# Performance work log

Measured on AMD Instinct MI355X. Metric: run time of the kernel, lower is better.

## Reference

```python
import jax, jax.numpy as jnp
import numpy as np

D_MODEL = 2048
N_HEADS = 16
D_HEAD = D_MODEL // N_HEADS  # 128
D_KV = 512
D_ROPE = 64
D_SPLIT = D_HEAD - D_ROPE  # 64
ROPE_BASE = 10000.0
EPS = 1e-5


def _rmsnorm(x, g):
    var = jnp.mean(x * x, axis=-1, keepdims=True) + EPS
    return g * (x * jax.lax.rsqrt(var))


def _rope_cache(seq):
    # theta over d_head frequencies, sliced to d_rope//2 then tiled x2 (as in source)
    half_rope = D_ROPE // 2
    theta = 1.0 / (ROPE_BASE ** (jnp.arange(0, D_HEAD, 2, dtype=jnp.float32) / D_HEAD))
    idx_theta = jnp.arange(seq, dtype=jnp.float32)[:, None] * theta[None, :]  # [seq, d_head//2]
    cos = jnp.tile(jnp.cos(idx_theta[:, :half_rope]), (1, 2))  # [seq, d_rope]
    sin = jnp.tile(jnp.sin(idx_theta[:, :half_rope]), (1, 2))
    return cos[None, :, None, :], sin[None, :, None, :]  # [1,seq,1,d_rope]


def _apply_rope(x, cos, sin):
    # NOTE: source does rot_x = cat(x.chunk(2,-1), -1) which is the identity,
    # so faithfully: x*cos + x*sin
    return x * cos + x * sin


def setup_inputs() -> dict:
    key = jax.random.key(0)
    ks = jax.random.split(key, 12)
    def w(k, i, o):
        return jax.random.normal(k, (i, o), dtype=jnp.float32) * (1.0 / np.sqrt(i))
    return {
        "x": jax.random.normal(ks[0], (2, 2048, D_MODEL), dtype=jnp.float32),
        "W_dq": w(ks[1], D_MODEL, D_KV),
        "W_uq": w(ks[2], D_KV, N_HEADS * D_SPLIT),
        "W_dkv": w(ks[3], D_MODEL, D_KV),
        "W_uk": w(ks[4], D_KV, N_HEADS * D_SPLIT),
        "W_uv": w(ks[5], D_KV, N_HEADS * D_HEAD),
        "W_qr": w(ks[6], D_KV, N_HEADS * D_ROPE),
        "W_kr": w(ks[7], D_MODEL, N_HEADS * D_ROPE),
        "g_q": jnp.ones((D_KV,), dtype=jnp.float32),
        "g_kv": jnp.ones((D_KV,), dtype=jnp.float32),
        "W_out": w(ks[8], D_MODEL, D_MODEL),
        "b_out": jnp.zeros((D_MODEL,), dtype=jnp.float32),
    }


def reference(x, W_dq, W_uq, W_dkv, W_uk, W_uv, W_qr, W_kr, g_q, g_kv, W_out, b_out):
    batch, seq, _ = x.shape
    cos, sin = _rope_cache(seq)

    c_q = _rmsnorm(x @ W_dq, g_q)                                   # [b,s,d_kv]
    q_base = (c_q @ W_uq).reshape(batch, seq, N_HEADS, D_SPLIT)
    q_rot = _apply_rope((c_q @ W_qr).reshape(batch, seq, N_HEADS, D_ROPE), cos, sin)

    c_kv = _rmsnorm(x @ W_dkv, g_kv)
    k_base = (c_kv @ W_uk).reshape(batch, seq, N_HEADS, D_SPLIT)
    k_rot = _apply_rope((x @ W_kr).reshape(batch, seq, N_HEADS, D_ROPE), cos, sin)
    v = (c_kv @ W_uv).reshape(batch, seq, N_HEADS, D_HEAD)

    q = jnp.concatenate([q_base, q_rot], axis=-1)                   # [b,s,h,d_head]
    k = jnp.concatenate([k_base, k_rot], axis=-1)

    scale = jnp.sqrt(jnp.float32(D_HEAD))
    scores = jnp.einsum('bnhd,bmhd->bhnm', q, k) / scale            # [b,h,s,s]
    causal = jnp.tril(jnp.ones((seq, seq), dtype=bool))
    scores = jnp.where(causal[None, None], scores, -jnp.inf)
    attn = jax.nn.softmax(scores, axis=-1)
    out = jnp.einsum('bhnm,bmhd->bnhd', attn, v)                    # [b,s,h,d_head]
    out = out.reshape(batch, seq, D_MODEL)
    return out @ W_out + b_out
```

## Files before the change

### kernel.cpp

```cpp
#include <hip/hip_runtime.h>
#include <hip/hip_bf16.h>
#include <cstdint>

typedef __bf16 v8bf __attribute__((ext_vector_type(8)));
typedef float  v4f  __attribute__((ext_vector_type(4)));

__device__ __forceinline__ unsigned short b16(float f) {
  union { float f; unsigned u; } v; v.f = f;
  unsigned u = v.u;
  return (unsigned short)((u + 0x7fffu + ((u >> 16) & 1u)) >> 16);
}
__device__ __forceinline__ float bf2f(unsigned short u) {
  union { unsigned u; float f; } v; v.u = ((unsigned)u) << 16; return v.f;
}

#define GLOAD_LDS16(g, l)                                                     \
  __builtin_amdgcn_global_load_lds(                                           \
      (const __attribute__((address_space(1))) void*)(g),                     \
      (__attribute__((address_space(3))) void*)(l), 16, 0, 0)

__global__ __launch_bounds__(256) void conv_bf16(const float* __restrict__ in,
                                                 unsigned short* __restrict__ out) {
  size_t idx = (size_t)blockIdx.x * 256 + threadIdx.x;
  v4f v = *(const v4f*)(in + idx * 4);
  unsigned long long p = (unsigned long long)b16(v[0]) |
                         ((unsigned long long)b16(v[1]) << 16) |
                         ((unsigned long long)b16(v[2]) << 32) |
                         ((unsigned long long)b16(v[3]) << 48);
  *(unsigned long long*)(out + idx * 4) = p;
}

__global__ void transpose_w(const float* __restrict__ in, unsigned short* __restrict__ out,
                            int C, int R) {
  __shared__ float tile[32][33];
  int c0 = blockIdx.x * 32, r0 = blockIdx.y * 32;
  int x = threadIdx.x, y = threadIdx.y;
#pragma unroll
  for (int i = 0; i < 4; ++i)
    tile[y + 8 * i][x] = in[(size_t)(r0 + y + 8 * i) * C + c0 + x];
  __syncthreads();
#pragma unroll
  for (int i = 0; i < 4; ++i)
    out[(size_t)(c0 + y + 8 * i) * R + r0 + x] = b16(tile[x][y + 8 * i]);
}

__global__ void transpose_v(const unsigned short* __restrict__ T3, unsigned short* __restrict__ VT) {
  __shared__ unsigned short tile[32][34];
  int bh = blockIdx.z;
  int s0 = blockIdx.x * 32, d0 = blockIdx.y * 32;
  int x = threadIdx.x, y = threadIdx.y;
  const unsigned short* src = T3 + (size_t)(bh >> 4) * 2048 * 3072 + 1024 + (bh & 15) * 128;
#pragma unroll
  for (int i = 0; i < 4; ++i)
    tile[y + 8 * i][x] = src[(size_t)(s0 + y + 8 * i) * 3072 + d0 + x];
  __syncthreads();
  unsigned short* dst = VT + (size_t)bh * 128 * 2048;
#pragma unroll
  for (int i = 0; i < 4; ++i)
    dst[(size_t)(d0 + y + 8 * i) * 2048 + s0 + x] = tile[x][y + 8 * i];
}

template <int MODE>
__global__ __launch_bounds__(256) void gemm_bt(const unsigned short* __restrict__ A,
                                               const unsigned short* __restrict__ BT,
                                               void* __restrict__ C0,
                                               void* __restrict__ C1,
                                               const float* __restrict__ bias,
                                               int M, int N, int K) {
  __shared__ unsigned short As[128 * 32];
  __shared__ unsigned short Bs[128 * 32];
  const int tid = threadIdx.x;
  const int w = tid >> 6, l = tid & 63;
  const int wm = w >> 1, wn = w & 1;
  const int lg = l >> 4, lr = l & 15;
  const int nwg = gridDim.x * gridDim.y;
  const int f = blockIdx.y * gridDim.x + blockIdx.x;
  const int swz = (f & 7) * (nwg >> 3) + (f >> 3);
  const int m0 = (swz / gridDim.x) * 128, n0 = (swz % gridDim.x) * 128;

  const int srow = tid >> 2, scol = (tid & 3) * 8;
  const unsigned short* Ap0 = A  + (size_t)(m0 + srow) * K + scol;
  const unsigned short* Ap1 = A  + (size_t)(m0 + 64 + srow) * K + scol;
  const unsigned short* Bp0 = BT + (size_t)(n0 + srow) * K + scol;
  const unsigned short* Bp1 = BT + (size_t)(n0 + 64 + srow) * K + scol;
  unsigned short* Ad0 = As + tid * 8;
  unsigned short* Ad1 = As + 2048 + tid * 8;
  unsigned short* Bd0 = Bs + tid * 8;
  unsigned short* Bd1 = Bs + 2048 + tid * 8;

  v4f acc[4][4];
#pragma unroll
  for (int i = 0; i < 4; ++i)
#pragma unroll
    for (int j = 0; j < 4; ++j) acc[i][j] = (v4f){0.f, 0.f, 0.f, 0.f};

  for (int k0 = 0; k0 < K; k0 += 32) {
    GLOAD_LDS16(Ap0 + k0, Ad0);
    GLOAD_LDS16(Ap1 + k0, Ad1);
    GLOAD_LDS16(Bp0 + k0, Bd0);
    GLOAD_LDS16(Bp1 + k0, Bd1);
    __syncthreads();
    v8bf af[4], bfr[4];
#pragma unroll
    for (int mi = 0; mi < 4; ++mi)
      af[mi] = *(const v8bf*)&As[(wm * 64 + mi * 16 + lr) * 32 + lg * 8];
#pragma unroll
    for (int ni = 0; ni < 4; ++ni)
      bfr[ni] = *(const v8bf*)&Bs[(wn * 64 + ni * 16 + lr) * 32 + lg * 8];
#pragma unroll
    for (int mi = 0; mi < 4; ++mi)
#pragma unroll
      for (int ni = 0; ni < 4; ++ni)
        acc[mi][ni] = __builtin_amdgcn_mfma_f32_16x16x32_bf16(af[mi], bfr[ni], acc[mi][ni], 0, 0, 0);
    __syncthreads();
  }
#pragma unroll
  for (int mi = 0; mi < 4; ++mi)
#pragma unroll
    for (int ni = 0; ni < 4; ++ni) {
      const int col = n0 + wn * 64 + ni * 16 + lr;
#pragma unroll
      for (int rr = 0; rr < 4; ++rr) {
        const int row = m0 + wm * 64 + mi * 16 + lg * 4 + rr;
        const float v = acc[mi][ni][rr];
        if (MODE == 0) {
          ((float*)C0)[(size_t)row * N + col] = v + bias[col];
        } else if (MODE == 1) {
          ((unsigned short*)C0)[(size_t)row * N + col] = b16(v);
        } else if (MODE == 2) {
          if (col < 1024) {
            int qc = (col >> 6) * 128 + (col & 63);
            ((unsigned short*)C0)[(size_t)row * 2048 + qc] = b16(v);
          } else {
            int cc = col - 1024, d = cc & 63;
            int qc = (cc >> 6) * 128 + 64 + d;
            int s = row & 2047;
            float ang = (float)s * __expf(-(float)(d & 31) * 0.14391156831f);
            float sn, cs; __sincosf(ang, &sn, &cs);
            ((unsigned short*)C0)[(size_t)row * 2048 + qc] = b16(v * (cs + sn));
          }
        } else {
          if (col < 1024) {
            int kc = (col >> 6) * 128 + (col & 63);
            ((unsigned short*)C0)[(size_t)row * 2048 + kc] = b16(v);
          } else {
            ((unsigned short*)C1)[(size_t)row * 3072 + col] = b16(v);
          }
        }
      }
    }
}

__global__ __launch_bounds__(256) void rmsnorm_rope(const unsigned short* __restrict__ T1,
                                                    const float* __restrict__ gq,
                                                    const float* __restrict__ gkv,
                                                    unsigned short* __restrict__ cq,
                                                    unsigned short* __restrict__ ckv,
                                                    unsigned short* __restrict__ Kb) {
  const int row = blockIdx.x;
  const int t = threadIdx.x;
  const int s = row & 2047;
  const unsigned short* rp = T1 + (size_t)row * 2048;
  float xq0 = bf2f(rp[t]), xq1 = bf2f(rp[256 + t]);
  float xk0 = bf2f(rp[512 + t]), xk1 = bf2f(rp[768 + t]);
  float sq = xq0 * xq0 + xq1 * xq1;
  float sk = xk0 * xk0 + xk1 * xk1;
#pragma unroll
  for (int o = 1; o < 64; o <<= 1) { sq += __shfl_xor(sq, o); sk += __shfl_xor(sk, o); }
  __shared__ float red[8];
  if ((t & 63) == 0) { red[t >> 6] = sq; red[4 + (t >> 6)] = sk; }
  __syncthreads();
  float rq = rsqrtf((red[0] + red[1] + red[2] + red[3]) * (1.f / 512.f) + 1e-5f);
  float rk = rsqrtf((red[4] + red[5] + red[6] + red[7]) * (1.f / 512.f) + 1e-5f);
  cq[(size_t)row * 512 + t]        = b16(gq[t] * xq0 * rq);
  cq[(size_t)row * 512 + 256 + t]  = b16(gq[256 + t] * xq1 * rq);
  ckv[(size_t)row * 512 + t]       = b16(gkv[t] * xk0 * rk);
  ckv[(size_t)row * 512 + 256 + t] = b16(gkv[256 + t] * xk1 * rk);
#pragma unroll
  for (int i = 0; i < 4; ++i) {
    int j = t + 256 * i;
    int hh = j >> 6, d = j & 63;
    float ang = (float)s * __expf(-(float)(d & 31) * 0.14391156831f);
    float sn, cs; __sincosf(ang, &sn, &cs);
    Kb[(size_t)row * 2048 + hh * 128 + 64 + d] = b16(bf2f(rp[1024 + j]) * (cs + sn));
  }
}

__global__ __launch_bounds__(256) void flash_attn(const unsigned short* __restrict__ Qb,
                                                  const unsigned short* __restrict__ Kb,
                                                  const unsigned short* __restrict__ VTb,
                                                  unsigned short* __restrict__ Ob) {
  __shared__ unsigned short Ks[64 * 128];
  __shared__ unsigned short Vs[128 * 64];
  __shared__ unsigned short Ps[4 * 16 * 72];
  const int b = blockIdx.z, h = blockIdx.y;
  const int pj = blockIdx.x;
  const int tid = threadIdx.x;
  const int w = tid >> 6, l = tid & 63;
  const int lg = l >> 4, lr = l & 15;
  const float scale = 0.0883883476483184f;

  const unsigned short* Kbase = Kb + (size_t)b * 2048 * 2048 + h * 128;
  const unsigned short* Vbase = VTb + (size_t)(b * 16 + h) * 128 * 2048;

  for (int pass = 0; pass < 2; ++pass) {
    const int q0 = (pass ? (31 - pj) : pj) * 64;
    const int qw0 = q0 + w * 16;

    v8bf qf[4];
    {
      const unsigned short* qp = Qb + (size_t)(b * 2048 + qw0 + lr) * 2048 + h * 128 + lg * 8;
#pragma unroll
      for (int ds = 0; ds < 4; ++ds) qf[ds] = *(const v8bf*)(qp + ds * 32);
    }
    v4f oacc[8];
#pragma unroll
    for (int i = 0; i < 8; ++i) oacc[i] = (v4f){0, 0, 0, 0};
    float mrow[4] = {-1e30f, -1e30f, -1e30f, -1e30f};
    float lsum[4] = {0, 0, 0, 0};

    const int nkv = q0 + 64;
    for (int kv0 = 0; kv0 < nkv; kv0 += 64) {
#pragma unroll
      for (int i = 0; i < 4; ++i) {
        int c = tid + 256 * i;
        int r = c >> 4, dbl = c & 15;
        int off = (r * 256 + dbl * 16) ^ ((r & 7) << 4);
        *(v4f*)((char*)Ks + off) =
            *(const v4f*)(Kbase + (size_t)(kv0 + r) * 2048 + dbl * 8);
      }
#pragma unroll
      for (int i = 0; i < 4; ++i) {
        int c = tid + 256 * i;
        int d = c >> 3, kbl = c & 7;
        int off = (d * 128 + kbl * 16) ^ ((d & 7) << 4);
        *(v4f*)((char*)Vs + off) =
            *(const v4f*)(Vbase + (size_t)d * 2048 + kv0 + kbl * 8);
      }
      __syncthreads();
      {
        float st[4][4];
        __builtin_amdgcn_s_setprio(1);
#pragma unroll
        for (int kt = 0; kt < 4; ++kt) {
          v4f sacc = (v4f){0, 0, 0, 0};
          int krow = kt * 16 + lr;
#pragma unroll
          for (int ds = 0; ds < 4; ++ds) {
            int off = (krow * 256 + ds * 64 + lg * 16) ^ ((krow & 7) << 4);
            v8bf kfr = *(const v8bf*)((char*)Ks + off);
            sacc = __builtin_amdgcn_mfma_f32_16x16x32_bf16(qf[ds], kfr, sacc, 0, 0, 0);
          }
          int colk = kv0 + kt * 16 + lr;
#pragma unroll
          for (int r = 0; r < 4; ++r) {
            int qrow = qw0 + lg * 4 + r;
            st[kt][r] = (colk <= qrow) ? sacc[r] * scale : -1e30f;
          }
        }
        __builtin_amdgcn_s_setprio(0);
#pragma unroll
        for (int r = 0; r < 4; ++r) {
          float mx = fmaxf(fmaxf(st[0][r], st[1][r]), fmaxf(st[2][r], st[3][r]));
#pragma unroll
          for (int o = 1; o < 16; o <<= 1) mx = fmaxf(mx, __shfl_xor(mx, o));
          float mnew = fmaxf(mrow[r], mx);
          float sc = __expf(mrow[r] - mnew);
          float ps = 0.f;
#pragma unroll
          for (int kt = 0; kt < 4; ++kt) {
            float p = __expf(st[kt][r] - mnew);
            ps += p;
            Ps[w * 1152 + (lg * 4 + r) * 72 + kt * 16 + lr] = b16(p);
          }
          lsum[r] = lsum[r] * sc + ps;
          mrow[r] = mnew;
#pragma unroll
          for (int dt = 0; dt < 8; ++dt) oacc[dt][r] *= sc;
        }
        __builtin_amdgcn_s_setprio(1);
#pragma unroll
        for (int kh = 0; kh < 2; ++kh) {
          v8bf pa = *(const v8bf*)((char*)Ps + w * 2304 + lr * 144 + kh * 64 + lg * 16);
#pragma unroll
          for (int dt = 0; dt < 8; ++dt) {
            int d = dt * 16 + lr;
            int off = (d * 128 + kh * 64 + lg * 16) ^ ((d & 7) << 4);
            v8bf vfr = *(const v8bf*)((char*)Vs + off);
            oacc[dt] = __builtin_amdgcn_mfma_f32_16x16x32_bf16(pa, vfr, oacc[dt], 0, 0, 0);
          }
        }
        __builtin_amdgcn_s_setprio(0);
      }
      __syncthreads();
    }
#pragma unroll
    for (int r = 0; r < 4; ++r) {
      float ls = lsum[r];
#pragma unroll
      for (int o = 1; o < 16; o <<= 1) ls += __shfl_xor(ls, o);
      float inv = 1.f / ls;
      size_t orow = (size_t)(b * 2048 + qw0 + lg * 4 + r) * 2048 + h * 128;
#pragma unroll
      for (int dt = 0; dt < 8; ++dt)
        Ob[orow + dt * 16 + lr] = b16(oacc[dt][r] * inv);
    }
  }
}

extern "C" void kernel_launch(void* const* d_in, const int* in_sizes, int n_in,
                              void* d_out, int out_size, void* d_ws, size_t ws_size,
                              hipStream_t stream) {
  const float* x    = (const float*)d_in[0];
  const float* Wdq  = (const float*)d_in[1];
  const float* Wuq  = (const float*)d_in[2];
  const float* Wdkv = (const float*)d_in[3];
  const float* Wuk  = (const float*)d_in[4];
  const float* Wuv  = (const float*)d_in[5];
  const float* Wqr  = (const float*)d_in[6];
  const float* Wkr  = (const float*)d_in[7];
  const float* gq   = (const float*)d_in[8];
  const float* gkv  = (const float*)d_in[9];
  const float* Wout = (const float*)d_in[10];
  const float* bout = (const float*)d_in[11];
  float* out = (float*)d_out;

  const size_t M1 = 1024 * 1024;
  unsigned short* xb  = (unsigned short*)d_ws;
  unsigned short* Qb  = xb;
  unsigned short* T   = xb + 8 * M1;
  unsigned short* Ob  = T;
  unsigned short* W1T = xb + 20 * M1;
  unsigned short* W2T = xb + 24 * M1;
  unsigned short* W3T = xb + 25 * M1;
  unsigned short* WoT = W3T + 1536 * 1024;
  unsigned short* cq  = xb + 30 * M1 + 512 * 1024;
  unsigned short* ckv = cq + 2 * M1;
  unsigned short* Kb = (unsigned short*)d_out;
  unsigned short* VT = Kb + 8 * M1;

  dim3 b256(256), tb(32, 8);

  conv_bf16<<<8192, b256, 0, stream>>>(x, xb);
  transpose_w<<<dim3(16, 64), tb, 0, stream>>>(Wdq,  W1T,                       512, 2048);
  transpose_w<<<dim3(16, 64), tb, 0, stream>>>(Wdkv, W1T + (size_t)512 * 2048,  512, 2048);
  transpose_w<<<dim3(32, 64), tb, 0, stream>>>(Wkr,  W1T + (size_t)1024 * 2048, 1024, 2048);
  transpose_w<<<dim3(32, 16), tb, 0, stream>>>(Wuq,  W2T,                       1024, 512);
  transpose_w<<<dim3(32, 16), tb, 0, stream>>>(Wqr,  W2T + (size_t)1024 * 512,  1024, 512);
  transpose_w<<<dim3(32, 16), tb, 0, stream>>>(Wuk,  W3T,                       1024, 512);
  transpose_w<<<dim3(64, 16), tb, 0, stream>>>(Wuv,  W3T + (size_t)1024 * 512,  2048, 512);
  transpose_w<<<dim3(64, 64), tb, 0, stream>>>(Wout, WoT,                       2048, 2048);

  gemm_bt<1><<<dim3(16, 32), b256, 0, stream>>>(xb, W1T, T, nullptr, nullptr, 4096, 2048, 2048);
  rmsnorm_rope<<<4096, b256, 0, stream>>>(T, gq, gkv, cq, ckv, Kb);
  gemm_bt<2><<<dim3(16, 32), b256, 0, stream>>>(cq, W2T, Qb, nullptr, nullptr, 4096, 2048, 512);
  gemm_bt<3><<<dim3(24, 32), b256, 0, stream>>>(ckv, W3T, Kb, T, nullptr, 4096, 3072, 512);
  transpose_v<<<dim3(64, 4, 32), tb, 0, stream>>>(T, VT);

  flash_attn<<<dim3(16, 16, 2), b256, 0, stream>>>(Qb, Kb, VT, Ob);

  gemm_bt<0><<<dim3(16, 32), b256, 0, stream>>>(Ob, WoT, out, nullptr, bout, 4096, 2048, 2048);
}
```

Before: 287.1 us.

## Merge Q and KV up-projection GEMMs and write V transposed in epilogue

The two up-projection GEMMs (Q and KV) are merged into one grouped launch with a swizzled block index that selects the operand set. The V part of the output is written directly in the transposed [b,h,d,s] layout through packed 64-bit stores, so the separate transpose_v kernel and its intermediate buffer round-trip are gone. This saves two kernel launches and one full pass over V. The cost is strided transposed stores from the GEMM epilogue.

```diff
diff --git a/kernel.cpp b/kernel.cpp
--- a/kernel.cpp
+++ b/kernel.cpp
@@ -44,27 +44,10 @@
     out[(size_t)(c0 + y + 8 * i) * R + r0 + x] = b16(tile[x][y + 8 * i]);
 }
 
-__global__ void transpose_v(const unsigned short* __restrict__ T3, unsigned short* __restrict__ VT) {
-  __shared__ unsigned short tile[32][34];
-  int bh = blockIdx.z;
-  int s0 = blockIdx.x * 32, d0 = blockIdx.y * 32;
-  int x = threadIdx.x, y = threadIdx.y;
-  const unsigned short* src = T3 + (size_t)(bh >> 4) * 2048 * 3072 + 1024 + (bh & 15) * 128;
-#pragma unroll
-  for (int i = 0; i < 4; ++i)
-    tile[y + 8 * i][x] = src[(size_t)(s0 + y + 8 * i) * 3072 + d0 + x];
-  __syncthreads();
-  unsigned short* dst = VT + (size_t)bh * 128 * 2048;
-#pragma unroll
-  for (int i = 0; i < 4; ++i)
-    dst[(size_t)(d0 + y + 8 * i) * 2048 + s0 + x] = tile[x][y + 8 * i];
-}
-
 template <int MODE>
 __global__ __launch_bounds__(256) void gemm_bt(const unsigned short* __restrict__ A,
                                                const unsigned short* __restrict__ BT,
                                                void* __restrict__ C0,
-                                               void* __restrict__ C1,
                                                const float* __restrict__ bias,
                                                int M, int N, int K) {
   __shared__ unsigned short As[128 * 32];
@@ -125,27 +108,111 @@
         const float v = acc[mi][ni][rr];
         if (MODE == 0) {
           ((float*)C0)[(size_t)row * N + col] = v + bias[col];
-        } else if (MODE == 1) {
+        } else {
           ((unsigned short*)C0)[(size_t)row * N + col] = b16(v);
-        } else if (MODE == 2) {
-          if (col < 1024) {
-            int qc = (col >> 6) * 128 + (col & 63);
-            ((unsigned short*)C0)[(size_t)row * 2048 + qc] = b16(v);
-          } else {
-            int cc = col - 1024, d = cc & 63;
-            int qc = (cc >> 6) * 128 + 64 + d;
-            int s = row & 2047;
+        }
+      }
+    }
+}
+
+__global__ __launch_bounds__(256) void gemm23(const unsigned short* __restrict__ cq,
+                                              const unsigned short* __restrict__ ckv,
+                                              const unsigned short* __restrict__ W2T,
+                                              const unsigned short* __restrict__ W3T,
+                                              unsigned short* __restrict__ Qb,
+                                              unsigned short* __restrict__ Kb,
+                                              unsigned short* __restrict__ VT) {
+  __shared__ unsigned short As[128 * 32];
+  __shared__ unsigned short Bs[128 * 32];
+  const int tid = threadIdx.x;
+  const int w = tid >> 6, l = tid & 63;
+  const int wm = w >> 1, wn = w & 1;
+  const int lg = l >> 4, lr = l & 15;
+  const int f = blockIdx.x;
+  const int swz = (f & 7) * 160 + (f >> 3);
+  const bool is3 = swz >= 512;
+  const int t = is3 ? swz - 512 : swz;
+  const int gx = is3 ? 24 : 16;
+  const int m0 = (t / gx) * 128, n0 = (t % gx) * 128;
+  const unsigned short* A  = is3 ? ckv : cq;
+  const unsigned short* BT = is3 ? W3T : W2T;
+  const int K = 512;
+
+  const int srow = tid >> 2, scol = (tid & 3) * 8;
+  const unsigned short* Ap0 = A  + (size_t)(m0 + srow) * K + scol;
+  const unsigned short* Ap1 = A  + (size_t)(m0 + 64 + srow) * K + scol;
+  const unsigned short* Bp0 = BT + (size_t)(n0 + srow) * K + scol;
+  const unsigned short* Bp1 = BT + (size_t)(n0 + 64 + srow) * K + scol;
+  unsigned short* Ad0 = As + tid * 8;
+  unsigned short* Ad1 = As + 2048 + tid * 8;
+  unsigned short* Bd0 = Bs + tid * 8;
+  unsigned short* Bd1 = Bs + 2048 + tid * 8;
+
+  v4f acc[4][4];
+#pragma unroll
+  for (int i = 0; i < 4; ++i)
+#pragma unroll
+    for (int j = 0; j < 4; ++j) acc[i][j] = (v4f){0.f, 0.f, 0.f, 0.f};
+
+  for (int k0 = 0; k0 < K; k0 += 32) {
+    GLOAD_LDS16(Ap0 + k0, Ad0);
+    GLOAD_LDS16(Ap1 + k0, Ad1);
+    GLOAD_LDS16(Bp0 + k0, Bd0);
+    GLOAD_LDS16(Bp1 + k0, Bd1);
+    __syncthreads();
+    v8bf af[4], bfr[4];
+#pragma unroll
+    for (int mi = 0; mi < 4; ++mi)
+      af[mi] = *(const v8bf*)&As[(wm * 64 + mi * 16 + lr) * 32 + lg * 8];
+#pragma unroll
+    for (int ni = 0; ni < 4; ++ni)
+      bfr[ni] = *(const v8bf*)&Bs[(wn * 64 + ni * 16 + lr) * 32 + lg * 8];
+#pragma unroll
+    for (int mi = 0; mi < 4; ++mi)
+#pragma unroll
+      for (int ni = 0; ni < 4; ++ni)
+        acc[mi][ni] = __builtin_amdgcn_mfma_f32_16x16x32_bf16(af[mi], bfr[ni], acc[mi][ni], 0, 0, 0);
+    __syncthreads();
+  }
+
+#pragma unroll
+  for (int mi = 0; mi < 4; ++mi)
+#pragma unroll
+    for (int ni = 0; ni < 4; ++ni) {
+      const int col = n0 + wn * 64 + ni * 16 + lr;
+      const int row0 = m0 + wm * 64 + mi * 16 + lg * 4;
+      if (!is3) {
+        if (col < 1024) {
+          int qc = (col >> 6) * 128 + (col & 63);
+#pragma unroll
+          for (int rr = 0; rr < 4; ++rr)
+            Qb[(size_t)(row0 + rr) * 2048 + qc] = b16(acc[mi][ni][rr]);
+        } else {
+          int cc = col - 1024, d = cc & 63;
+          int qc = (cc >> 6) * 128 + 64 + d;
+#pragma unroll
+          for (int rr = 0; rr < 4; ++rr) {
+            int s = (row0 + rr) & 2047;
             float ang = (float)s * __expf(-(float)(d & 31) * 0.14391156831f);
             float sn, cs; __sincosf(ang, &sn, &cs);
-            ((unsigned short*)C0)[(size_t)row * 2048 + qc] = b16(v * (cs + sn));
+            Qb[(size_t)(row0 + rr) * 2048 + qc] = b16(acc[mi][ni][rr] * (cs + sn));
           }
+        }
+      } else {
+        if (col < 1024) {
+          int kc = (col >> 6) * 128 + (col & 63);
+#pragma unroll
+          for (int rr = 0; rr < 4; ++rr)
+            Kb[(size_t)(row0 + rr) * 2048 + kc] = b16(acc[mi][ni][rr]);
         } else {
-          if (col < 1024) {
-            int kc = (col >> 6) * 128 + (col & 63);
-            ((unsigned short*)C0)[(size_t)row * 2048 + kc] = b16(v);
-          } else {
-            ((unsigned short*)C1)[(size_t)row * 3072 + col] = b16(v);
-          }
+          int hd = col - 1024, h = hd >> 7, d = hd & 127;
+          int b = row0 >> 11, s = row0 & 2047;
+          unsigned long long p =
+              (unsigned long long)b16(acc[mi][ni][0]) |
+              ((unsigned long long)b16(acc[mi][ni][1]) << 16) |
+              ((unsigned long long)b16(acc[mi][ni][2]) << 32) |
+              ((unsigned long long)b16(acc[mi][ni][3]) << 48);
+          *(unsigned long long*)&VT[(size_t)((b * 16 + h) * 128 + d) * 2048 + s] = p;
         }
       }
     }
@@ -351,13 +418,11 @@
   transpose_w<<<dim3(64, 16), tb, 0, stream>>>(Wuv,  W3T + (size_t)1024 * 512,  2048, 512);
   transpose_w<<<dim3(64, 64), tb, 0, stream>>>(Wout, WoT,                       2048, 2048);
 
-  gemm_bt<1><<<dim3(16, 32), b256, 0, stream>>>(xb, W1T, T, nullptr, nullptr, 4096, 2048, 2048);
+  gemm_bt<1><<<dim3(16, 32), b256, 0, stream>>>(xb, W1T, T, nullptr, 4096, 2048, 2048);
   rmsnorm_rope<<<4096, b256, 0, stream>>>(T, gq, gkv, cq, ckv, Kb);
-  gemm_bt<2><<<dim3(16, 32), b256, 0, stream>>>(cq, W2T, Qb, nullptr, nullptr, 4096, 2048, 512);
-  gemm_bt<3><<<dim3(24, 32), b256, 0, stream>>>(ckv, W3T, Kb, T, nullptr, 4096, 3072, 512);
-  transpose_v<<<dim3(64, 4, 32), tb, 0, stream>>>(T, VT);
+  gemm23<<<dim3(1280), b256, 0, stream>>>(cq, ckv, W2T, W3T, Qb, Kb, VT);
 
   flash_attn<<<dim3(16, 16, 2), b256, 0, stream>>>(Qb, Kb, VT, Ob);
 
-  gemm_bt<0><<<dim3(16, 32), b256, 0, stream>>>(Ob, WoT, out, nullptr, bout, 4096, 2048, 2048);
-}
+  gemm_bt<0><<<dim3(16, 32), b256, 0, stream>>>(Ob, WoT, out, bout, 4096, 2048, 2048);
+}
```

Result: faster. 280.8 us (-2.2%).
